# Performance work log

Hardware: AMD Instinct MI355X
Metric: run time of the kernel (lower is better)

The kernel has to match this reference:

```python
import jax, jax.numpy as jnp
from jax import lax
import numpy as np

S, N, E = 4, 50000, 800000
D_IN, D_NOISE, D_H, D_OUT = 96, 32, 32, 128
F_CAT = D_IN + D_NOISE + D_H  # 160, matches nn.Linear(input_dim+noise_dim+32, out)


def setup_inputs() -> dict:
    key = jax.random.key(0)
    ks = jax.random.split(key, 8)
    X = jax.random.normal(ks[0], (1, N, D_IN), dtype=jnp.float32)
    h = jax.random.normal(ks[1], (1, N, D_H), dtype=jnp.float32)
    # Bernoulli(0.5) noise, sampled in setup for determinism (original samples in forward)
    epsilon = (jax.random.uniform(ks[2], (S, N, D_NOISE)) < 0.5).astype(jnp.float32)
    W = jax.random.normal(ks[3], (F_CAT, D_OUT), dtype=jnp.float32) * 0.02
    b = jnp.zeros((D_OUT,), dtype=jnp.float32)
    gin_eps = jnp.zeros((), dtype=jnp.float32)  # init_eps=0, learn_eps=True
    src = jax.random.randint(ks[4], (E,), 0, N, dtype=jnp.int32)
    dst = jax.random.randint(ks[5], (E,), 0, N, dtype=jnp.int32)
    return {"X": X, "h": h, "epsilon": epsilon, "W": W, "b": b,
            "gin_eps": gin_eps, "src": src, "dst": dst}


def reference(X, h, epsilon, W, b, gin_eps, src, dst):
    # X: [1,N,D_IN] expanded to sample_size; h: [1,N,32] expanded; epsilon: [S,N,D_NOISE]
    s, n = epsilon.shape[0], X.shape[1]
    Xb = jnp.broadcast_to(X, (s, n, X.shape[2]))
    hb = jnp.broadcast_to(h, (s, n, h.shape[2]))
    x_all = jnp.concatenate([Xb, epsilon, hb], axis=2)  # [S,N,F_CAT]

    def per_sample(carry, x):  # x: [N,F_CAT]
        # GINConv('sum'): (1+eps)*x + sum_{j in N(i)} x_j, then Linear, then activation
        agg = (1.0 + gin_eps) * x + jax.ops.segment_sum(x[src], dst, num_segments=n)
        y = jax.nn.relu(agg @ W + b)           # [N,D_OUT]
        return carry, jnp.mean(y, axis=0)      # per-layer mean over nodes -> [D_OUT]

    _, means = lax.scan(per_sample, None, x_all)  # [S,D_OUT]
    # outputTensor[i] = tempdim12 broadcasts the [D_OUT] vector over the node axis
    out = jnp.broadcast_to(means[:, None, :], (s, n, W.shape[1]))
    return jax.nn.relu(out), epsilon
```

## Files before the change

### kernel.cpp

```cpp
#include <hip/hip_runtime.h>

#define N_NODES  50000
#define N_EDGES  800000
#define D_OUTF   128
#define F_PACK   256
#define NTILES   3125
#define GEMM_BLOCKS 512
#define NB1      196

typedef __attribute__((ext_vector_type(8))) short bf16x8;
typedef __attribute__((ext_vector_type(4))) float f32x4;

__device__ __forceinline__ unsigned short f2bf(float x) {
  unsigned int u = __float_as_uint(x);
  u += 0x7FFFu + ((u >> 16) & 1u);
  return (unsigned short)(u >> 16);
}
__device__ __forceinline__ float bflo(unsigned int u) { return __uint_as_float(u << 16); }
__device__ __forceinline__ float bfhi(unsigned int u) { return __uint_as_float(u & 0xFFFF0000u); }
__device__ __forceinline__ unsigned int pack2(float a, float b) {
  return (unsigned int)f2bf(a) | ((unsigned int)f2bf(b) << 16);
}

__global__ void k_pack_xh(const float* __restrict__ X, const float* __restrict__ h,
                          unsigned int* __restrict__ featXH) {
  int t = blockIdx.x * blockDim.x + threadIdx.x;
  if (t >= N_NODES * 64) return;
  int node = t >> 6, f = (t & 63) << 1;
  float a, c;
  if (f < 96) { a = X[node * 96 + f];      c = X[node * 96 + f + 1]; }
  else        { a = h[node * 32 + f - 96]; c = h[node * 32 + f - 95]; }
  featXH[t] = pack2(a, c);
}

__global__ void k_pack_bits(const float* __restrict__ eps, unsigned int* __restrict__ epsb) {
  long g = (long)blockIdx.x * blockDim.x + threadIdx.x;
  if (g >= (long)4 * N_NODES * 32) return;
  float v = eps[g];
  unsigned long long m = __ballot(v > 0.5f);
  int lane = threadIdx.x & 63;
  if ((lane & 31) == 0) {
    long idx = g >> 5;
    int s = (int)(idx / N_NODES);
    int node = (int)(idx - (long)s * N_NODES);
    epsb[node * 4 + s] = (unsigned int)(m >> ((lane >> 5) * 32));
  }
}

__global__ void k_hist(const int* __restrict__ dst, int* __restrict__ cnt) {
  int i = blockIdx.x * blockDim.x + threadIdx.x;
  if (i < N_EDGES) atomicAdd(&cnt[dst[i]], 1);
}

__global__ void k_scan1(const int* __restrict__ cnt, int* __restrict__ excl,
                        int* __restrict__ bsum) {
  __shared__ int wpart[4];
  int tid = threadIdx.x, lane = tid & 63, wid = tid >> 6;
  int i = blockIdx.x * 256 + tid;
  int v = (i < N_NODES) ? cnt[i] : 0;
  int x = v;
#pragma unroll
  for (int d = 1; d < 64; d <<= 1) {
    int t = __shfl_up(x, d, 64);
    if (lane >= d) x += t;
  }
  if (lane == 63) wpart[wid] = x;
  __syncthreads();
  if (tid == 0) {
    int s = 0;
#pragma unroll
    for (int w = 0; w < 4; ++w) { int t = wpart[w]; wpart[w] = s; s += t; }
    bsum[blockIdx.x] = s;
  }
  __syncthreads();
  if (i < N_NODES) excl[i] = wpart[wid] + x - v;
}

__global__ void k_scan2(const int* __restrict__ bsum, int* __restrict__ boff) {
  __shared__ int sd[256];
  int tid = threadIdx.x;
  int v = (tid < NB1) ? bsum[tid] : 0;
  sd[tid] = v;
  __syncthreads();
  for (int d = 1; d < 256; d <<= 1) {
    int t = (tid >= d) ? sd[tid - d] : 0;
    __syncthreads();
    sd[tid] += t;
    __syncthreads();
  }
  if (tid < NB1) boff[tid] = sd[tid] - v;
}

__global__ void k_scan3(int* __restrict__ off, const int* __restrict__ boff,
                        int* __restrict__ cursor) {
  int i = blockIdx.x * 256 + threadIdx.x;
  if (i < N_NODES) {
    int o = off[i] + boff[blockIdx.x];
    off[i] = o;
    cursor[i] = o;
  }
  if (i == 0) off[N_NODES] = N_EDGES;
}

__global__ void k_scatter(const int* __restrict__ src, const int* __restrict__ dst,
                          int* __restrict__ cursor, int* __restrict__ csr) {
  int i = blockIdx.x * blockDim.x + threadIdx.x;
  if (i < N_EDGES) {
    int pos = atomicAdd(&cursor[dst[i]], 1);
    csr[pos] = src[i];
  }
}

__device__ __forceinline__ unsigned int selw(uint4 b, int widx) {
  return widx == 0 ? b.x : widx == 1 ? b.y : widx == 2 ? b.z : b.w;
}

__global__ __launch_bounds__(256) void k_agg(const unsigned int* __restrict__ featXH,
                      const uint4* __restrict__ epsb,
                      const float* __restrict__ geps_p,
                      const int* __restrict__ off, const int* __restrict__ csr,
                      unsigned int* __restrict__ agg_u) {
  int wave = (blockIdx.x * blockDim.x + threadIdx.x) >> 6;
  int lane = threadIdx.x & 63;
  if (wave >= N_NODES) return;
  int n = wave;
  float ge = 1.0f + geps_p[0];
  int widx = lane >> 4, sh = (2 * lane) & 31;

  unsigned int su = featXH[n * 64 + lane];
  float a0 = ge * bflo(su), a1 = ge * bfhi(su);
  unsigned int sw = selw(epsb[n], widx);
  float e0 = ge * (float)((sw >> sh) & 1u);
  float e1 = ge * (float)((sw >> (sh + 1)) & 1u);
  int c0 = 0, c1 = 0;

  int e = off[n], eend = off[n + 1];
  for (; e + 1 < eend; e += 2) {
    int s0 = csr[e], s1 = csr[e + 1];
    unsigned int u0 = featXH[s0 * 64 + lane];
    unsigned int u1 = featXH[s1 * 64 + lane];
    uint4 b0 = epsb[s0];
    uint4 b1 = epsb[s1];
    a0 += bflo(u0); a1 += bfhi(u0);
    a0 += bflo(u1); a1 += bfhi(u1);
    unsigned int w0 = selw(b0, widx), w1 = selw(b1, widx);
    c0 += (int)((w0 >> sh) & 1u) + (int)((w1 >> sh) & 1u);
    c1 += (int)((w0 >> (sh + 1)) & 1u) + (int)((w1 >> (sh + 1)) & 1u);
  }
  if (e < eend) {
    int s0 = csr[e];
    unsigned int u0 = featXH[s0 * 64 + lane];
    uint4 b0 = epsb[s0];
    a0 += bflo(u0); a1 += bfhi(u0);
    unsigned int w0 = selw(b0, widx);
    c0 += (int)((w0 >> sh) & 1u);
    c1 += (int)((w0 >> (sh + 1)) & 1u);
  }
  e0 += (float)c0; e1 += (float)c1;

  unsigned int* ar = agg_u + n * 128;
  ar[lane]      = pack2(a0, a1);
  ar[64 + lane] = pack2(e0, e1);
}

__global__ __launch_bounds__(256) void k_gemm(const unsigned short* __restrict__ agg,
    const float* __restrict__ W, const float* __restrict__ b,
    float* __restrict__ partials) {
  int tid = threadIdx.x;
  int lane = tid & 63;
  int w = tid >> 6;
  int col = lane & 15;
  int quad = lane >> 4;

  bf16x8 Bsh[2][4];
  bf16x8 Bep[2];
  float bias[2];
#pragma unroll
  for (int i = 0; i < 2; ++i) {
    int obase = (2 * w + i) * 16;
    bias[i] = b[obase + col];
#pragma unroll
    for (int kb = 0; kb < 4; ++kb) {
      bf16x8 f;
#pragma unroll
      for (int j = 0; j < 8; ++j) {
        int k = kb * 32 + quad * 8 + j;
        int wr = (k < 96) ? k : k + 32;
        f[j] = (short)f2bf(W[wr * D_OUTF + obase + col]);
      }
      Bsh[i][kb] = f;
    }
    bf16x8 g;
#pragma unroll
    for (int j = 0; j < 8; ++j)
      g[j] = (short)f2bf(W[(96 + quad * 8 + j) * D_OUTF + obase + col]);
    Bep[i] = g;
  }

  f32x4 psum[4][2];
#pragma unroll
  for (int s = 0; s < 4; ++s)
#pragma unroll
    for (int i = 0; i < 2; ++i) psum[s][i] = (f32x4){0.f, 0.f, 0.f, 0.f};

  for (int t = blockIdx.x; t < NTILES; t += gridDim.x) {
    const unsigned short* arow = agg + (long)(t * 16 + col) * F_PACK;
    bf16x8 Ash[4];
#pragma unroll
    for (int kb = 0; kb < 4; ++kb)
      Ash[kb] = *(const bf16x8*)(arow + kb * 32 + quad * 8);
    f32x4 csh[2];
    csh[0] = (f32x4){0.f, 0.f, 0.f, 0.f};
    csh[1] = (f32x4){0.f, 0.f, 0.f, 0.f};
#pragma unroll
    for (int kb = 0; kb < 4; ++kb) {
      csh[0] = __builtin_amdgcn_mfma_f32_16x16x32_bf16(Ash[kb], Bsh[0][kb], csh[0], 0, 0, 0);
      csh[1] = __builtin_amdgcn_mfma_f32_16x16x32_bf16(Ash[kb], Bsh[1][kb], csh[1], 0, 0, 0);
    }
#pragma unroll
    for (int s = 0; s < 4; ++s) {
      bf16x8 Aep = *(const bf16x8*)(arow + 128 + s * 32 + quad * 8);
#pragma unroll
      for (int i = 0; i < 2; ++i) {
        f32x4 c = __builtin_amdgcn_mfma_f32_16x16x32_bf16(Aep, Bep[i], csh[i], 0, 0, 0);
#pragma unroll
        for (int r = 0; r < 4; ++r)
          psum[s][i][r] += fmaxf(c[r] + bias[i], 0.f);
      }
    }
  }

#pragma unroll
  for (int s = 0; s < 4; ++s)
#pragma unroll
    for (int i = 0; i < 2; ++i) {
      float v = psum[s][i][0] + psum[s][i][1] + psum[s][i][2] + psum[s][i][3];
      v += __shfl_xor(v, 16, 64);
      v += __shfl_xor(v, 32, 64);
      if (quad == 0)
        partials[blockIdx.x * 512 + s * 128 + (2 * w + i) * 16 + col] = v;
    }
}

__global__ void k_reduce(const float* __restrict__ partials, float* __restrict__ means) {
  int idx = blockIdx.x * 64 + threadIdx.x;
  float t = 0.f;
  for (int blk = 0; blk < GEMM_BLOCKS; ++blk) t += partials[blk * 512 + idx];
  means[idx] = fmaxf(t * (1.0f / (float)N_NODES), 0.f);
}

#define OUT0_F4 6400000L
#define EPS_F4  1600000L
__global__ void k_out(const float* __restrict__ means, const float* __restrict__ eps,
                      float* __restrict__ out) {
  long i = (long)blockIdx.x * blockDim.x + threadIdx.x;
  if (i < OUT0_F4) {
    int o4 = (int)(i & 31);
    long sn = i >> 5;
    int s = (int)(sn / N_NODES);
    ((float4*)out)[i] = ((const float4*)means)[s * 32 + o4];
  } else if (i < OUT0_F4 + EPS_F4) {
    long j = i - OUT0_F4;
    ((float4*)out)[OUT0_F4 + j] = ((const float4*)eps)[j];
  }
}

extern "C" void kernel_launch(void* const* d_in, const int* in_sizes, int n_in,
                              void* d_out, int out_size, void* d_ws, size_t ws_size,
                              hipStream_t stream) {
  const float* X    = (const float*)d_in[0];
  const float* h    = (const float*)d_in[1];
  const float* eps  = (const float*)d_in[2];
  const float* W    = (const float*)d_in[3];
  const float* b    = (const float*)d_in[4];
  const float* geps = (const float*)d_in[5];
  const int*   src  = (const int*)d_in[6];
  const int*   dst  = (const int*)d_in[7];
  float* out = (float*)d_out;

  char* w = (char*)d_ws;
  unsigned int*  featXH = (unsigned int*)w;  w += (size_t)N_NODES * 64 * 4;
  unsigned int*  epsb   = (unsigned int*)w;  w += (size_t)N_NODES * 4 * 4;
  unsigned int*  agg_u  = (unsigned int*)w;  w += (size_t)N_NODES * 128 * 4;
  int*   off      = (int*)w;   w += (size_t)(N_NODES + 16) * 4;
  int*   cnt      = (int*)w;   w += (size_t)N_NODES * 4;
  int*   cursor   = (int*)w;   w += (size_t)N_NODES * 4;
  int*   csr      = (int*)w;   w += (size_t)N_EDGES * 4;
  int*   bsum     = (int*)w;   w += 256 * 4;
  int*   boff     = (int*)w;   w += 256 * 4;
  float* partials = (float*)w; w += (size_t)GEMM_BLOCKS * 512 * 4;
  float* means    = (float*)w; w += 512 * 4;

  hipMemsetAsync(cnt, 0, (size_t)N_NODES * 4, stream);

  int eb = (N_EDGES + 255) / 256;
  k_pack_xh<<<(N_NODES * 64 + 255) / 256, 256, 0, stream>>>(X, h, featXH);
  k_pack_bits<<<(4 * N_NODES * 32 + 255) / 256, 256, 0, stream>>>(eps, epsb);
  k_hist<<<eb, 256, 0, stream>>>(dst, cnt);
  k_scan1<<<NB1, 256, 0, stream>>>(cnt, off, bsum);
  k_scan2<<<1, 256, 0, stream>>>(bsum, boff);
  k_scan3<<<NB1, 256, 0, stream>>>(off, boff, cursor);
  k_scatter<<<eb, 256, 0, stream>>>(src, dst, cursor, csr);

  k_agg<<<(N_NODES + 3) / 4, 256, 0, stream>>>(featXH, (const uint4*)epsb, geps, off, csr, agg_u);

  k_gemm<<<GEMM_BLOCKS, 256, 0, stream>>>((const unsigned short*)agg_u, W, b, partials);
  k_reduce<<<8, 64, 0, stream>>>(partials, means);

  long total_f4 = OUT0_F4 + EPS_F4;
  k_out<<<(int)((total_f4 + 255) / 256), 256, 0, stream>>>(means, eps, out);
}
```

Baseline: 397.8 us.

## Aggregate each node with 16 lanes using 128-bit feature loads

Replaces the one-wave-per-node aggregation kernel with one that maps 16 threads to each node, so each wave processes four nodes. Each thread loads a uint4 (8 bf16 features) and one byte of the epsilon bitmask per neighbor, and writes the output with 128-bit stores. This cuts wasted lanes and per-node instruction overhead and widens memory transactions. In exchange it drops the two-edge unroll and uses more registers per thread, and it adds divergence within a wave when the four nodes have different degrees.

```diff
diff --git a/kernel.cpp b/kernel.cpp
--- a/kernel.cpp
+++ b/kernel.cpp
@@ -20,6 +20,9 @@
 __device__ __forceinline__ float bfhi(unsigned int u) { return __uint_as_float(u & 0xFFFF0000u); }
 __device__ __forceinline__ unsigned int pack2(float a, float b) {
   return (unsigned int)f2bf(a) | ((unsigned int)f2bf(b) << 16);
+}
+__device__ __forceinline__ unsigned int selw(uint4 b, int widx) {
+  return widx == 0 ? b.x : widx == 1 ? b.y : widx == 2 ? b.z : b.w;
 }
 
 __global__ void k_pack_xh(const float* __restrict__ X, const float* __restrict__ h,
@@ -111,56 +114,56 @@
   }
 }
 
-__device__ __forceinline__ unsigned int selw(uint4 b, int widx) {
-  return widx == 0 ? b.x : widx == 1 ? b.y : widx == 2 ? b.z : b.w;
-}
-
-__global__ __launch_bounds__(256) void k_agg(const unsigned int* __restrict__ featXH,
-                      const uint4* __restrict__ epsb,
-                      const float* __restrict__ geps_p,
-                      const int* __restrict__ off, const int* __restrict__ csr,
-                      unsigned int* __restrict__ agg_u) {
-  int wave = (blockIdx.x * blockDim.x + threadIdx.x) >> 6;
-  int lane = threadIdx.x & 63;
-  if (wave >= N_NODES) return;
-  int n = wave;
+__global__ __launch_bounds__(256) void k_agg16(
+    const uint4* __restrict__ feat4, const uint4* __restrict__ epsb,
+    const float* __restrict__ geps_p, const int* __restrict__ off,
+    const int* __restrict__ csr, uint4* __restrict__ agg4) {
+  int gt = blockIdx.x * blockDim.x + threadIdx.x;
+  int n  = gt >> 4;
+  int li = gt & 15;
+  if (n >= N_NODES) return;
   float ge = 1.0f + geps_p[0];
-  int widx = lane >> 4, sh = (2 * lane) & 31;
-
-  unsigned int su = featXH[n * 64 + lane];
-  float a0 = ge * bflo(su), a1 = ge * bfhi(su);
-  unsigned int sw = selw(epsb[n], widx);
-  float e0 = ge * (float)((sw >> sh) & 1u);
-  float e1 = ge * (float)((sw >> (sh + 1)) & 1u);
-  int c0 = 0, c1 = 0;
-
-  int e = off[n], eend = off[n + 1];
-  for (; e + 1 < eend; e += 2) {
-    int s0 = csr[e], s1 = csr[e + 1];
-    unsigned int u0 = featXH[s0 * 64 + lane];
-    unsigned int u1 = featXH[s1 * 64 + lane];
-    uint4 b0 = epsb[s0];
-    uint4 b1 = epsb[s1];
-    a0 += bflo(u0); a1 += bfhi(u0);
-    a0 += bflo(u1); a1 += bfhi(u1);
-    unsigned int w0 = selw(b0, widx), w1 = selw(b1, widx);
-    c0 += (int)((w0 >> sh) & 1u) + (int)((w1 >> sh) & 1u);
-    c1 += (int)((w0 >> (sh + 1)) & 1u) + (int)((w1 >> (sh + 1)) & 1u);
-  }
-  if (e < eend) {
+  int wsel = li >> 2, bsh = (li & 3) * 8;
+
+  uint4 sf = feat4[n * 16 + li];
+  float af0 = ge * bflo(sf.x), af1 = ge * bfhi(sf.x);
+  float af2 = ge * bflo(sf.y), af3 = ge * bfhi(sf.y);
+  float af4 = ge * bflo(sf.z), af5 = ge * bfhi(sf.z);
+  float af6 = ge * bflo(sf.w), af7 = ge * bfhi(sf.w);
+  unsigned int Bself = (selw(epsb[n], wsel) >> bsh) & 0xFFu;
+  int c0 = 0, c1 = 0, c2 = 0, c3 = 0, c4 = 0, c5 = 0, c6 = 0, c7 = 0;
+
+  int e = off[n], e1 = off[n + 1];
+  for (; e < e1; ++e) {
     int s0 = csr[e];
-    unsigned int u0 = featXH[s0 * 64 + lane];
-    uint4 b0 = epsb[s0];
-    a0 += bflo(u0); a1 += bfhi(u0);
-    unsigned int w0 = selw(b0, widx);
-    c0 += (int)((w0 >> sh) & 1u);
-    c1 += (int)((w0 >> (sh + 1)) & 1u);
-  }
-  e0 += (float)c0; e1 += (float)c1;
-
-  unsigned int* ar = agg_u + n * 128;
-  ar[lane]      = pack2(a0, a1);
-  ar[64 + lane] = pack2(e0, e1);
+    uint4 f0 = feat4[s0 * 16 + li];
+    unsigned int B0 = (selw(epsb[s0], wsel) >> bsh) & 0xFFu;
+    af0 += bflo(f0.x); af1 += bfhi(f0.x);
+    af2 += bflo(f0.y); af3 += bfhi(f0.y);
+    af4 += bflo(f0.z); af5 += bfhi(f0.z);
+    af6 += bflo(f0.w); af7 += bfhi(f0.w);
+    c0 += (int)(B0 & 1u);        c1 += (int)((B0 >> 1) & 1u);
+    c2 += (int)((B0 >> 2) & 1u); c3 += (int)((B0 >> 3) & 1u);
+    c4 += (int)((B0 >> 4) & 1u); c5 += (int)((B0 >> 5) & 1u);
+    c6 += (int)((B0 >> 6) & 1u); c7 += (int)((B0 >> 7) & 1u);
+  }
+
+  float ev0 = ge * (float)(Bself & 1u)        + (float)c0;
+  float ev1 = ge * (float)((Bself >> 1) & 1u) + (float)c1;
+  float ev2 = ge * (float)((Bself >> 2) & 1u) + (float)c2;
+  float ev3 = ge * (float)((Bself >> 3) & 1u) + (float)c3;
+  float ev4 = ge * (float)((Bself >> 4) & 1u) + (float)c4;
+  float ev5 = ge * (float)((Bself >> 5) & 1u) + (float)c5;
+  float ev6 = ge * (float)((Bself >> 6) & 1u) + (float)c6;
+  float ev7 = ge * (float)((Bself >> 7) & 1u) + (float)c7;
+
+  uint4 oXh, oEp;
+  oXh.x = pack2(af0, af1); oXh.y = pack2(af2, af3);
+  oXh.z = pack2(af4, af5); oXh.w = pack2(af6, af7);
+  oEp.x = pack2(ev0, ev1); oEp.y = pack2(ev2, ev3);
+  oEp.z = pack2(ev4, ev5); oEp.w = pack2(ev6, ev7);
+  agg4[n * 32 + li]      = oXh;
+  agg4[n * 32 + 16 + li] = oEp;
 }
 
 __global__ __launch_bounds__(256) void k_gemm(const unsigned short* __restrict__ agg,
@@ -302,7 +305,8 @@
   k_scan3<<<NB1, 256, 0, stream>>>(off, boff, cursor);
   k_scatter<<<eb, 256, 0, stream>>>(src, dst, cursor, csr);
 
-  k_agg<<<(N_NODES + 3) / 4, 256, 0, stream>>>(featXH, (const uint4*)epsb, geps, off, csr, agg_u);
+  k_agg16<<<NTILES, 256, 0, stream>>>((const uint4*)featXH, (const uint4*)epsb,
+                                      geps, off, csr, (uint4*)agg_u);
 
   k_gemm<<<GEMM_BLOCKS, 256, 0, stream>>>((const unsigned short*)agg_u, W, b, partials);
   k_reduce<<<8, 64, 0, stream>>>(partials, means);
```

Result: faster. 377.9 us (-5.0%).
